# Optimization experiments

Hardware: AMD Instinct MI355X
Metric: run time of the kernel (lower is better)

The kernel has to match this reference:

```python
import jax, jax.numpy as jnp
import numpy as np

B, H, W, C, NH = 16, 56, 56, 192, 6
N = H * W
HD = C // NH
EPS = 1e-5


def _ln(x, g, b):
    m = jnp.mean(x, -1, keepdims=True)
    v = jnp.mean((x - m) ** 2, -1, keepdims=True)
    return (x - m) * jax.lax.rsqrt(v + EPS) * g + b


def _dwconv(x, w, b):
    # x: (B,H,W,Ch), w: (3,3,1,Ch) depthwise, SAME padding
    y = jax.lax.conv_general_dilated(
        x, w, (1, 1), 'SAME',
        dimension_numbers=('NHWC', 'HWIO', 'NHWC'),
        feature_group_count=x.shape[-1])
    return y + b


def _rope_tables():
    k_max = C // 4  # 2D RoPE: feature_dim // (2 * num_spatial_dims)
    theta = 1.0 / (10000.0 ** (jnp.arange(k_max, dtype=jnp.float32) / k_max))
    ai = jnp.arange(H, dtype=jnp.float32)[:, None, None] * theta
    aj = jnp.arange(W, dtype=jnp.float32)[None, :, None] * theta
    ang = jnp.concatenate([jnp.broadcast_to(ai, (H, W, k_max)),
                           jnp.broadcast_to(aj, (H, W, k_max))], -1)  # (H,W,C//2)
    return jnp.cos(ang), jnp.sin(ang)


def _rope(x, cos, sin):
    # x: (B,H,W,C); complex multiply on interleaved (re,im) pairs
    xr, xi = x[..., 0::2], x[..., 1::2]
    return jnp.stack([cos * xr - sin * xi, cos * xi + sin * xr], -1).reshape(x.shape)


def reference(x, cpe1_w, cpe1_b, norm1_g, norm1_b, in_w, in_b, actp_w, actp_b,
              dwc_w, dwc_b, qk_w, qk_b, lepe_w, lepe_b, outp_w, outp_b,
              cpe2_w, cpe2_b, norm2_g, norm2_b, fc1_w, fc1_b, mdw_w, mdw_b,
              fc2_w, fc2_b, mn1_g, mn1_b, mn2_g, mn2_b, mn3_g, mn3_b):
    img = lambda t: t.reshape(B, H, W, -1)
    seq = lambda t: t.reshape(B, N, -1)

    # CPE1
    x = x + seq(_dwconv(img(x), cpe1_w, cpe1_b))
    shortcut = x
    xn = _ln(x, norm1_g, norm1_b)

    # gated branch
    act_res = jax.nn.silu(xn @ actp_w + actp_b)
    h = seq(jax.nn.silu(_dwconv(img(xn @ in_w + in_b), dwc_w, dwc_b)))

    # --- LinearAttention (ELU+1 kernel, RoPE, LePE) ---
    qk = h @ qk_w + qk_b                      # (B,N,2C)
    q = jax.nn.elu(qk[..., :C]) + 1.0
    k = jax.nn.elu(qk[..., C:]) + 1.0
    cos, sin = _rope_tables()
    q_r = seq(_rope(img(q), cos, sin)).reshape(B, N, NH, HD)
    k_r = seq(_rope(img(k), cos, sin)).reshape(B, N, NH, HD)
    q4 = q.reshape(B, N, NH, HD)
    k4 = k.reshape(B, N, NH, HD)
    v4 = h.reshape(B, N, NH, HD)
    kmean = jnp.mean(k4, axis=1)                                  # (B,NH,HD)
    z = 1.0 / (jnp.einsum('bnhd,bhd->bnh', q4, kmean) + 1e-6)     # (B,N,NH)
    kv = jnp.einsum('bnhd,bnhe->bhde', k_r, v4) / N               # (B,NH,HD,HD)
    attn = jnp.einsum('bnhd,bhde->bnhe', q_r, kv) * z[..., None]
    attn = attn.reshape(B, N, C)
    attn = attn + seq(_dwconv(img(h), lepe_w, lepe_b))            # LePE on v

    x = shortcut + (attn * act_res) @ outp_w + outp_b

    # CPE2
    x = x + seq(_dwconv(img(x), cpe2_w, cpe2_b))

    # FRN MLP: fc1 -> dwconv -> 3 chained residual LayerNorms -> GELU -> fc2
    xm = _ln(x, norm2_g, norm2_b)
    f1 = xm @ fc1_w + fc1_b                   # (B,N,768)
    dw = seq(_dwconv(img(f1), mdw_w, mdw_b))
    n1 = _ln(dw + f1, mn1_g, mn1_b)
    n2 = _ln(n1 + f1, mn2_g, mn2_b)
    n3 = _ln(n2 + f1, mn3_g, mn3_b)
    x = x + jax.nn.gelu(n3, approximate=False) @ fc2_w + fc2_b
    return x


def setup_inputs() -> dict:
    key = jax.random.key(0)
    cnt = [0]
    def rn(shape, s=0.05):
        cnt[0] += 1
        return jax.random.normal(jax.random.fold_in(key, cnt[0]), shape, jnp.float32) * s
    dws = (3, 3, 1, C)
    z = lambda n: jnp.zeros((n,), jnp.float32)
    o = lambda n: jnp.ones((n,), jnp.float32)
    return dict(
        x=rn((B, N, C), 1.0),
        cpe1_w=rn(dws), cpe1_b=z(C),
        norm1_g=o(C), norm1_b=z(C),
        in_w=rn((C, C)), in_b=z(C),
        actp_w=rn((C, C)), actp_b=z(C),
        dwc_w=rn(dws), dwc_b=z(C),
        qk_w=rn((C, 2 * C)), qk_b=z(2 * C),
        lepe_w=rn(dws), lepe_b=z(C),
        outp_w=rn((C, C)), outp_b=z(C),
        cpe2_w=rn(dws), cpe2_b=z(C),
        norm2_g=o(C), norm2_b=z(C),
        fc1_w=rn((C, 4 * C)), fc1_b=z(4 * C),
        mdw_w=rn((3, 3, 1, 4 * C)), mdw_b=z(4 * C),
        fc2_w=rn((4 * C, C)), fc2_b=z(C),
        mn1_g=o(4 * C), mn1_b=z(4 * C),
        mn2_g=o(4 * C), mn2_b=z(4 * C),
        mn3_g=o(4 * C), mn3_b=z(4 * C),
    )
```

## Files before the change

kernel.cpp:

```cpp
#include <hip/hip_runtime.h>
#include <hip/hip_bf16.h>
#include <math.h>

#define BB 16
#define HH 56
#define WW 56
#define CC0 192
#define NHH 6
#define HDD 32
#define NPOS (HH*WW)
#define MROWS (BB*NPOS)
#define C4 (4*CC0)

typedef __hip_bfloat16 bf16;
typedef short short8 __attribute__((ext_vector_type(8)));
typedef short short4v __attribute__((ext_vector_type(4)));
typedef float f32x4 __attribute__((ext_vector_type(4)));
typedef float f32x2 __attribute__((ext_vector_type(2)));
typedef unsigned int u32;
typedef u32 u32x4 __attribute__((ext_vector_type(4)));
typedef u32 u32x2 __attribute__((ext_vector_type(2)));

__device__ __forceinline__ float b2f(bf16 v){ return __bfloat162float(v); }
__device__ __forceinline__ bf16 f2b(float v){ return __float2bfloat16(v); }
__device__ __forceinline__ short f2s(float v){ bf16 b = __float2bfloat16(v); return *(short*)&b; }
__device__ __forceinline__ float s2f(short s){ bf16 b; *(short*)&b = s; return __bfloat162float(b); }
__device__ __forceinline__ f32x2 bfp(u32 u){
  union { u32 q; float f; } lo, hi;
  lo.q = u << 16; hi.q = u & 0xffff0000u;
  return (f32x2){lo.f, hi.f};
}
__device__ __forceinline__ float fast_gelu(float x){
  float u = 1.5957691216f * (x + 0.044715f*x*x*x);
  float t = 1.f - 2.f/(__expf(u) + 1.f);
  return 0.5f*x*(1.f + t);
}
__device__ __forceinline__ int swz8(int bid, int nblk){
  return (bid & 7) * (nblk >> 3) + (bid >> 3);
}

__global__ __launch_bounds__(256) void convert_weights(
    const float* __restrict__ w0, const float* __restrict__ w1,
    const float* __restrict__ w2, const float* __restrict__ w3,
    const float* __restrict__ w4, const float* __restrict__ w5,
    short* __restrict__ dst){
  int t = blockIdx.x*256 + threadIdx.x;
  int e = t*4;
  if (e >= 479232) return;
  const float* src; int K, N, off;
  if      (e <  36864){ src=w0; K=192; N=192; off=0; }
  else if (e <  73728){ src=w1; K=192; N=192; off=36864; }
  else if (e < 147456){ src=w2; K=192; N=384; off=73728; }
  else if (e < 184320){ src=w3; K=192; N=192; off=147456; }
  else if (e < 331776){ src=w4; K=192; N=768; off=184320; }
  else                { src=w5; K=768; N=192; off=331776; }
  int le = e - off;
  int n = le / K, k = le % K;
  short4v o;
  #pragma unroll
  for (int l = 0; l < 4; ++l) o[l] = f2s(src[(size_t)(k+l)*N + n]);
  *(short4v*)(dst + e) = o;
}

__global__ __launch_bounds__(256) void cpe_ln_kernel(const float* __restrict__ in,
    const float* __restrict__ w, const float* __restrict__ bias,
    const float* __restrict__ g, const float* __restrict__ bb,
    float* __restrict__ x1out, bf16* __restrict__ xnout){
  int wv = threadIdx.x >> 6, lane = threadIdx.x & 63;
  int grp = swz8(blockIdx.x, gridDim.x)*4 + wv;
  int pos0 = grp * 4;
  int b = pos0 / NPOS; int ij = pos0 % NPOS; int i = ij / WW; int j0 = ij % WW;
  int c = lane * 3;
  float acc[4][3];
  {
    float b0 = bias[c], b1 = bias[c+1], b2 = bias[c+2];
    #pragma unroll
    for (int p = 0; p < 4; ++p){ acc[p][0]=b0; acc[p][1]=b1; acc[p][2]=b2; }
  }
  float fc[4][3];
  bool leftOK  = (j0 > 0);
  bool rightOK = (j0 + 4 < WW);
  int base_i = (b*NPOS + i*WW + j0)*CC0 + c;

  #pragma unroll
  for (int di = 0; di < 3; ++di){
    int ii = i + di - 1;
    if (ii < 0 || ii >= HH) continue;
    int rb = base_i + (di-1)*(WW*CC0);
    float wt[3][3];
    #pragma unroll
    for (int dj = 0; dj < 3; ++dj){
      const float* wp = w + (di*3 + dj)*CC0 + c;
      wt[dj][0] = wp[0]; wt[dj][1] = wp[1]; wt[dj][2] = wp[2];
    }
    if (leftOK){
      const float* ip = in + rb - CC0;
      float d0 = ip[0], d1 = ip[1], d2 = ip[2];
      acc[0][0] += d0*wt[0][0]; acc[0][1] += d1*wt[0][1]; acc[0][2] += d2*wt[0][2];
    }
    #pragma unroll
    for (int col = 1; col <= 4; ++col){
      const float* ip = in + rb + (col-1)*CC0;
      float d0 = ip[0], d1 = ip[1], d2 = ip[2];
      if (di == 1){ fc[col-1][0] = d0; fc[col-1][1] = d1; fc[col-1][2] = d2; }
      #pragma unroll
      for (int dj = 0; dj < 3; ++dj){
        int p = col - dj;
        if (p >= 0 && p < 4){
          acc[p][0] += d0*wt[dj][0]; acc[p][1] += d1*wt[dj][1]; acc[p][2] += d2*wt[dj][2];
        }
      }
    }
    if (rightOK){
      const float* ip = in + rb + 4*CC0;
      float d0 = ip[0], d1 = ip[1], d2 = ip[2];
      acc[3][0] += d0*wt[2][0]; acc[3][1] += d1*wt[2][1]; acc[3][2] += d2*wt[2][2];
    }
  }
  float gv0 = g[c], gv1 = g[c+1], gv2 = g[c+2];
  float bv0 = bb[c], bv1 = bb[c+1], bv2 = bb[c+2];
  #pragma unroll
  for (int p = 0; p < 4; ++p){
    float v0 = fc[p][0] + acc[p][0];
    float v1 = fc[p][1] + acc[p][1];
    float v2 = fc[p][2] + acc[p][2];
    int base = (pos0 + p)*CC0 + c;
    float* xp = x1out + base;
    xp[0] = v0; xp[1] = v1; xp[2] = v2;
    float s = v0+v1+v2, q = v0*v0+v1*v1+v2*v2;
    #pragma unroll
    for (int m = 1; m < 64; m <<= 1){ s += __shfl_xor(s, m, 64); q += __shfl_xor(q, m, 64); }
    float mean = s * (1.f/CC0);
    float rstd = rsqrtf(q * (1.f/CC0) - mean*mean + 1e-5f);
    bf16* op = xnout + base;
    op[0] = f2b((v0-mean)*rstd*gv0 + bv0);
    op[1] = f2b((v1-mean)*rstd*gv1 + bv1);
    op[2] = f2b((v2-mean)*rstd*gv2 + bv2);
  }
}

template<typename TIN, int CC, int MODE>
__global__ __launch_bounds__(256) void dwconv_v(const TIN* __restrict__ in,
    const float* __restrict__ w, const float* __restrict__ bias, void* __restrict__ out){
  constexpr int VEC = 16 / (int)sizeof(TIN);
  constexpr int NG = CC / VEC;
  int idx = swz8(blockIdx.x, gridDim.x)*256 + threadIdx.x;
  int cg = idx % NG; int pos = idx / NG;
  int b = pos / NPOS; int ij = pos % NPOS; int i = ij / WW; int j = ij % WW;
  int cb = cg * VEC;
  float acc[VEC];
  #pragma unroll
  for (int l = 0; l < VEC; ++l) acc[l] = bias[cb + l];
  #pragma unroll
  for (int di = 0; di < 3; ++di){
    int ii = i + di - 1;
    if (ii < 0 || ii >= HH) continue;
    #pragma unroll
    for (int dj = 0; dj < 3; ++dj){
      int jj = j + dj - 1;
      if (jj < 0 || jj >= WW) continue;
      int off = (b*NPOS + ii*WW + jj)*CC + cb;
      const float* wp = w + (di*3 + dj)*CC + cb;
      short8 v = *(const short8*)((const short*)in + off);
      #pragma unroll
      for (int l = 0; l < 8; ++l) acc[l] += s2f(v[l]) * wp[l];
    }
  }
  int oidx = pos*CC + cb;
  if constexpr (MODE == 1){
    short8 o;
    #pragma unroll
    for (int l = 0; l < 8; ++l){ float s = acc[l]/(1.f + expf(-acc[l])); o[l] = f2s(s); }
    *(short8*)((short*)out + oidx) = o;
  } else {
    short* op = (short*)out + oidx;
    short8 r = *(short8*)op;
    short8 o;
    #pragma unroll
    for (int l = 0; l < 8; ++l) o[l] = f2s(s2f(r[l]) + acc[l]);
    *(short8*)op = o;
  }
}

#define BM 256
#define BN 64
#define BK 32
#define LDA 40
template<int K, int N, int ALOAD, int EPI>
__global__ __launch_bounds__(256) void mfma_gemm(
    const void* __restrict__ a0v, const void* __restrict__ a1v,
    const short* __restrict__ wT, const float* __restrict__ bias,
    const float* __restrict__ addf, void* __restrict__ out0, void* __restrict__ out1){
  __shared__ short As[BM*LDA];
  __shared__ short Bs[BN*LDA];
  int tid = threadIdx.x;
  int wave = tid >> 6, lane = tid & 63;
  size_t m0 = (size_t)blockIdx.x * BM;
  int n0 = blockIdx.y * BN;
  int wm = wave * 64;
  int am = lane & 15, ak = (lane >> 4) * 8;

  f32x4 acc[4][4];
  #pragma unroll
  for (int mt = 0; mt < 4; ++mt)
    #pragma unroll
    for (int nt = 0; nt < 4; ++nt)
      acc[mt][nt] = (f32x4){0.f,0.f,0.f,0.f};

  for (int k0 = 0; k0 < K; k0 += BK){
    if constexpr (ALOAD == 0){
      const short* A = (const short*)a0v;
      #pragma unroll
      for (int it = 0; it < 4; ++it){
        int idx = it*256 + tid;
        int row = idx >> 2; int ko = (idx & 3) * 8;
        short8 v = *(const short8*)(A + (m0 + row)*(size_t)K + k0 + ko);
        *(short8*)&As[row*LDA + ko] = v;
      }
    } else {
      const short* A0p = (const short*)a0v;
      const short* A1p = (const short*)a1v;
      #pragma unroll
      for (int it = 0; it < 4; ++it){
        int idx = it*256 + tid;
        int row = idx >> 2; int ko = (idx & 3) * 8;
        size_t off = (m0 + row)*(size_t)K + k0 + ko;
        short8 va = *(const short8*)(A0p + off);
        short8 vb = *(const short8*)(A1p + off);
        short8 o;
        #pragma unroll
        for (int l = 0; l < 8; ++l) o[l] = f2s(s2f(va[l]) * s2f(vb[l]));
        *(short8*)&As[row*LDA + ko] = o;
      }
    }
    {
      int row = tid >> 2; int ko = (tid & 3) * 8;
      short8 v = *(const short8*)(wT + (size_t)(n0 + row)*K + k0 + ko);
      *(short8*)&Bs[row*LDA + ko] = v;
    }
    __syncthreads();
    short8 af[4], bfr[4];
    #pragma unroll
    for (int mt = 0; mt < 4; ++mt) af[mt] = *(short8*)&As[(wm + mt*16 + am)*LDA + ak];
    #pragma unroll
    for (int nt = 0; nt < 4; ++nt) bfr[nt] = *(short8*)&Bs[(nt*16 + am)*LDA + ak];
    #pragma unroll
    for (int mt = 0; mt < 4; ++mt)
      #pragma unroll
      for (int nt = 0; nt < 4; ++nt)
        acc[mt][nt] = __builtin_amdgcn_mfma_f32_16x16x32_bf16(af[mt], bfr[nt], acc[mt][nt], 0, 0, 0);
    __syncthreads();
  }

  int cn = lane & 15;
  int cr = (lane >> 4) * 4;
  #pragma unroll
  for (int mt = 0; mt < 4; ++mt){
    #pragma unroll
    for (int nt = 0; nt < 4; ++nt){
      int gn = n0 + nt*16 + cn;
      float bv = bias[gn];
      #pragma unroll
      for (int r = 0; r < 4; ++r){
        size_t gm = m0 + wm + mt*16 + cr + r;
        float v = acc[mt][nt][r] + bv;
        if constexpr (EPI == 0){
          ((bf16*)out0)[gm*N + gn] = f2b(v);
        } else if constexpr (EPI == 1){
          ((bf16*)out0)[gm*N + gn] = f2b(v / (1.f + expf(-v)));
        } else if constexpr (EPI == 2){
          float rv = (v > 0.f) ? (v + 1.f) : expf(v);
          if (n0 < CC0) ((bf16*)out0)[gm*CC0 + gn] = f2b(rv);
          else          ((bf16*)out1)[gm*CC0 + (gn - CC0)] = f2b(rv);
        } else {
          ((float*)out0)[gm*N + gn] = addf[gm*N + gn] + v;
        }
      }
    }
  }
}

__global__ void rope_tables_kernel(float* __restrict__ cosT, float* __restrict__ sinT){
  int idx = blockIdx.x*256 + threadIdx.x;
  if (idx >= NPOS*96) return;
  int t = idx % 96; int ij = idx / 96; int i = ij / WW; int j = ij % WW;
  int kk = (t < 48) ? t : (t - 48);
  float th = expf(-(float)kk * 0.19188209108283716f);
  float pos = (t < 48) ? (float)i : (float)j;
  float ang = pos * th;
  cosT[idx] = cosf(ang);
  sinT[idx] = sinf(ang);
}

__global__ __launch_bounds__(CC0) void kmean_kernel(const bf16* __restrict__ k, float* __restrict__ kmean){
  int b = blockIdx.x / 28; int chunk = blockIdx.x % 28; int c = threadIdx.x;
  const bf16* kp = k + ((size_t)b*NPOS + (size_t)chunk*112)*CC0 + c;
  float s0 = 0.f, s1 = 0.f, s2 = 0.f, s3 = 0.f;
  #pragma unroll 1
  for (int r = 0; r < 112; r += 4){
    s0 += b2f(kp[(size_t)(r+0)*CC0]);
    s1 += b2f(kp[(size_t)(r+1)*CC0]);
    s2 += b2f(kp[(size_t)(r+2)*CC0]);
    s3 += b2f(kp[(size_t)(r+3)*CC0]);
  }
  atomicAdd(&kmean[b*CC0 + c], (s0+s1+s2+s3) * (1.f/NPOS));
}

#define KVCH 14
__global__ __launch_bounds__(256) void kv_kernel(const bf16* __restrict__ kbuf,
    const bf16* __restrict__ hbuf, const float* __restrict__ cosT,
    const float* __restrict__ sinT, float* __restrict__ kv){
  int bi = blockIdx.x;
  int chunk = bi % KVCH; bi /= KVCH;
  int h = bi % NHH; int b = bi / NHH;
  int tid = threadIdx.x;
  int r8 = tid >> 5, lane = tid & 31;
  __shared__ float krs[8][32];
  __shared__ float vvs[8][32];
  int d = tid >> 3; int ebase = (tid & 7) * 4;
  float a0 = 0.f, a1 = 0.f, a2 = 0.f, a3 = 0.f;
  int c = h*HDD + lane;
  int t = c >> 1;
  bool odd = (lane & 1);
  for (int step = 0; step < NPOS/(KVCH*8); ++step){
    int n = chunk*(NPOS/KVCH) + step*8 + r8;
    size_t row = (size_t)b*NPOS + n;
    float kc = b2f(kbuf[row*CC0 + c]);
    float kp = b2f(kbuf[row*CC0 + (c ^ 1)]);
    float cs = cosT[(size_t)n*96 + t], sn = sinT[(size_t)n*96 + t];
    krs[r8][lane] = odd ? (cs*kc + sn*kp) : (cs*kc - sn*kp);
    vvs[r8][lane] = b2f(hbuf[row*CC0 + c]);
    __syncthreads();
    #pragma unroll
    for (int nn = 0; nn < 8; ++nn){
      float kk2 = krs[nn][d];
      a0 += kk2 * vvs[nn][ebase+0];
      a1 += kk2 * vvs[nn][ebase+1];
      a2 += kk2 * vvs[nn][ebase+2];
      a3 += kk2 * vvs[nn][ebase+3];
    }
    __syncthreads();
  }
  const float invN = 1.f/NPOS;
  float* kvp = kv + (((size_t)(b*NHH + h)*HDD + d)*HDD) + ebase;
  atomicAdd(kvp+0, a0*invN);
  atomicAdd(kvp+1, a1*invN);
  atomicAdd(kvp+2, a2*invN);
  atomicAdd(kvp+3, a3*invN);
}

__global__ __launch_bounds__(CC0) void attn_kernel(const bf16* __restrict__ q,
    const float* __restrict__ kmean, const float* __restrict__ kv,
    const float* __restrict__ cosT, const float* __restrict__ sinT,
    bf16* __restrict__ out){
  int row = blockIdx.x;
  int tid = threadIdx.x;
  int b = row / NPOS; int n = row % NPOS;
  __shared__ float qs[CC0];
  __shared__ float qrs[NHH*33];
  __shared__ float zsh[NHH];
  qs[tid] = b2f(q[(size_t)row*CC0 + tid]);
  __syncthreads();
  float pm = qs[tid] * kmean[b*CC0 + tid];
  #pragma unroll
  for (int m = 16; m >= 1; m >>= 1) pm += __shfl_xor(pm, m, 32);
  if ((tid & 31) == 0) zsh[tid >> 5] = 1.f/(pm + 1e-6f);
  int t = tid >> 1;
  float cs = cosT[(size_t)n*96 + t], sn = sinT[(size_t)n*96 + t];
  float qr = (tid & 1) ? (cs*qs[tid] + sn*qs[tid-1]) : (cs*qs[tid] - sn*qs[tid+1]);
  int hh = tid >> 5, d = tid & 31;
  qrs[hh*33 + d] = qr;
  __syncthreads();
  const float* kvp = kv + (size_t)(b*NHH + hh)*HDD*HDD;
  float acc = 0.f;
  #pragma unroll
  for (int d2 = 0; d2 < HDD; ++d2) acc += qrs[hh*33 + d2] * kvp[d2*HDD + d];
  out[(size_t)row*CC0 + tid] = f2b(acc * zsh[hh]);
}

__global__ __launch_bounds__(256) void mdw_ln_kernel(const bf16* __restrict__ f1,
    const float* __restrict__ w, const float* __restrict__ bias,
    const float* __restrict__ g1, const float* __restrict__ b1,
    const float* __restrict__ g2, const float* __restrict__ b2,
    const float* __restrict__ g3, const float* __restrict__ b3,
    bf16* __restrict__ out){
  int wv = threadIdx.x >> 6, lane = threadIdx.x & 63;
  int grp = swz8(blockIdx.x, gridDim.x)*4 + wv;
  int pos0 = grp * 4;
  int b = pos0 / NPOS; int ij = pos0 % NPOS; int i = ij / WW; int j0 = ij % WW;
  int c0 = lane * 8;
  int c1 = 512 + lane * 4;
  const short* fp = (const short*)f1;

  f32x2 acc2[4][6];
  {
    f32x2 bv[6];
    #pragma unroll
    for (int l = 0; l < 4; ++l) bv[l] = *(const f32x2*)(bias + c0 + 2*l);
    bv[4] = *(const f32x2*)(bias + c1);
    bv[5] = *(const f32x2*)(bias + c1 + 2);
    #pragma unroll
    for (int p = 0; p < 4; ++p)
      #pragma unroll
      for (int l = 0; l < 6; ++l) acc2[p][l] = bv[l];
  }
  u32x4 fca[4]; u32x2 fcb[4];
  bool leftOK  = (j0 > 0);
  bool rightOK = (j0 + 4 < WW);
  int base_i = (b*NPOS + i*WW + j0)*C4;

  #pragma unroll
  for (int di = 0; di < 3; ++di){
    int ii = i + di - 1;
    if (ii < 0 || ii >= HH) continue;
    int rb = base_i + (di-1)*(WW*C4);
    f32x2 wt2[3][6];
    #pragma unroll
    for (int dj = 0; dj < 3; ++dj){
      const float* wp = w + (di*3 + dj)*C4;
      #pragma unroll
      for (int l = 0; l < 4; ++l) wt2[dj][l] = *(const f32x2*)(wp + c0 + 2*l);
      wt2[dj][4] = *(const f32x2*)(wp + c1);
      wt2[dj][5] = *(const f32x2*)(wp + c1 + 2);
    }
    if (leftOK){
      u32x4 xa = *(const u32x4*)(fp + rb - C4 + c0);
      u32x2 xb = *(const u32x2*)(fp + rb - C4 + c1);
      f32x2 dv[6];
      dv[0]=bfp(xa[0]); dv[1]=bfp(xa[1]); dv[2]=bfp(xa[2]); dv[3]=bfp(xa[3]);
      dv[4]=bfp(xb[0]); dv[5]=bfp(xb[1]);
      #pragma unroll
      for (int l = 0; l < 6; ++l) acc2[0][l] += dv[l]*wt2[0][l];
    }
    #pragma unroll
    for (int col = 1; col <= 4; ++col){
      int off = rb + (col-1)*C4;
      u32x4 xa = *(const u32x4*)(fp + off + c0);
      u32x2 xb = *(const u32x2*)(fp + off + c1);
      if (di == 1){ fca[col-1] = xa; fcb[col-1] = xb; }
      f32x2 dv[6];
      dv[0]=bfp(xa[0]); dv[1]=bfp(xa[1]); dv[2]=bfp(xa[2]); dv[3]=bfp(xa[3]);
      dv[4]=bfp(xb[0]); dv[5]=bfp(xb[1]);
      #pragma unroll
      for (int dj = 0; dj < 3; ++dj){
        int p = col - dj;
        if (p >= 0 && p < 4){
          #pragma unroll
          for (int l = 0; l < 6; ++l) acc2[p][l] += dv[l]*wt2[dj][l];
        }
      }
    }
    if (rightOK){
      u32x4 xa = *(const u32x4*)(fp + rb + 4*C4 + c0);
      u32x2 xb = *(const u32x2*)(fp + rb + 4*C4 + c1);
      f32x2 dv[6];
      dv[0]=bfp(xa[0]); dv[1]=bfp(xa[1]); dv[2]=bfp(xa[2]); dv[3]=bfp(xa[3]);
      dv[4]=bfp(xb[0]); dv[5]=bfp(xb[1]);
      #pragma unroll
      for (int l = 0; l < 6; ++l) acc2[3][l] += dv[l]*wt2[2][l];
    }
  }
  #pragma unroll
  for (int p = 0; p < 4; ++p){
    #pragma unroll
    for (int l = 0; l < 4; ++l) acc2[p][l] += bfp(fca[p][l]);
    acc2[p][4] += bfp(fcb[p][0]);
    acc2[p][5] += bfp(fcb[p][1]);
  }

  const float* gs[3] = {g1, g2, g3};
  const float* bs[3] = {b1, b2, b3};
  #pragma unroll
  for (int pass = 0; pass < 3; ++pass){
    f32x2 gv[6], bvv[6];
    #pragma unroll
    for (int l = 0; l < 4; ++l){
      gv[l]  = *(const f32x2*)(gs[pass] + c0 + 2*l);
      bvv[l] = *(const f32x2*)(bs[pass] + c0 + 2*l);
    }
    gv[4]  = *(const f32x2*)(gs[pass] + c1);  gv[5]  = *(const f32x2*)(gs[pass] + c1 + 2);
    bvv[4] = *(const f32x2*)(bs[pass] + c1);  bvv[5] = *(const f32x2*)(bs[pass] + c1 + 2);
    #pragma unroll
    for (int p = 0; p < 4; ++p){
      f32x2 s2 = acc2[p][0];
      f32x2 q2 = acc2[p][0]*acc2[p][0];
      #pragma unroll
      for (int l = 1; l < 6; ++l){ s2 += acc2[p][l]; q2 += acc2[p][l]*acc2[p][l]; }
      float s = s2[0]+s2[1], q = q2[0]+q2[1];
      #pragma unroll
      for (int m = 1; m < 64; m <<= 1){ s += __shfl_xor(s, m, 64); q += __shfl_xor(q, m, 64); }
      float mean = s * (1.f/C4);
      float rstd = rsqrtf(q * (1.f/C4) - mean*mean + 1e-5f);
      #pragma unroll
      for (int l = 0; l < 6; ++l){
        f32x2 rg = gv[l]*rstd;
        f32x2 t  = acc2[p][l] - mean;
        acc2[p][l] = t*rg + bvv[l];
      }
      if (pass < 2){
        #pragma unroll
        for (int l = 0; l < 4; ++l) acc2[p][l] += bfp(fca[p][l]);
        acc2[p][4] += bfp(fcb[p][0]);
        acc2[p][5] += bfp(fcb[p][1]);
      }
    }
  }
  #pragma unroll
  for (int p = 0; p < 4; ++p){
    short8 o0; short4v o1;
    #pragma unroll
    for (int l = 0; l < 4; ++l){
      o0[2*l]   = f2s(fast_gelu(acc2[p][l][0]));
      o0[2*l+1] = f2s(fast_gelu(acc2[p][l][1]));
    }
    o1[0] = f2s(fast_gelu(acc2[p][4][0]));
    o1[1] = f2s(fast_gelu(acc2[p][4][1]));
    o1[2] = f2s(fast_gelu(acc2[p][5][0]));
    o1[3] = f2s(fast_gelu(acc2[p][5][1]));
    int ob = (pos0 + p)*C4;
    *(short8*)((short*)out + ob + c0) = o0;
    *(short4v*)((short*)out + ob + c1) = o1;
  }
}

extern "C" void kernel_launch(void* const* d_in, const int* in_sizes, int n_in,
                              void* d_out, int out_size, void* d_ws, size_t ws_size,
                              hipStream_t stream){
  (void)in_sizes; (void)n_in; (void)out_size; (void)ws_size;
  const float* X      = (const float*)d_in[0];
  const float* cpe1_w = (const float*)d_in[1];
  const float* cpe1_b = (const float*)d_in[2];
  const float* n1g    = (const float*)d_in[3];
  const float* n1b    = (const float*)d_in[4];
  const float* in_w   = (const float*)d_in[5];
  const float* in_b   = (const float*)d_in[6];
  const float* actp_w = (const float*)d_in[7];
  const float* actp_b = (const float*)d_in[8];
  const float* dwc_w  = (const float*)d_in[9];
  const float* dwc_b  = (const float*)d_in[10];
  const float* qk_w   = (const float*)d_in[11];
  const float* qk_b   = (const float*)d_in[12];
  const float* lepe_w = (const float*)d_in[13];
  const float* lepe_b = (const float*)d_in[14];
  const float* outp_w = (const float*)d_in[15];
  const float* outp_b = (const float*)d_in[16];
  const float* cpe2_w = (const float*)d_in[17];
  const float* cpe2_b = (const float*)d_in[18];
  const float* n2g    = (const float*)d_in[19];
  const float* n2b    = (const float*)d_in[20];
  const float* fc1_w  = (const float*)d_in[21];
  const float* fc1_b  = (const float*)d_in[22];
  const float* mdw_w  = (const float*)d_in[23];
  const float* mdw_b  = (const float*)d_in[24];
  const float* fc2_w  = (const float*)d_in[25];
  const float* fc2_b  = (const float*)d_in[26];
  const float* mn1g   = (const float*)d_in[27];
  const float* mn1b   = (const float*)d_in[28];
  const float* mn2g   = (const float*)d_in[29];
  const float* mn2b   = (const float*)d_in[30];
  const float* mn3g   = (const float*)d_in[31];
  const float* mn3b   = (const float*)d_in[32];

  char* ws = (char*)d_ws;
  const size_t SZF = (size_t)MROWS*CC0*4;
  const size_t SZB = (size_t)MROWS*CC0*2;
  float* A0 = (float*)(ws);
  char* base2 = ws + SZF;
  bf16* BQ = (bf16*)(base2 + 0*SZB);
  bf16* BKb= (bf16*)(base2 + 1*SZB);
  bf16* BA = (bf16*)(base2 + 2*SZB);
  bf16* B1 = (bf16*)(base2 + 3*SZB);
  bf16* B0 = (bf16*)(base2 + 4*SZB);
  bf16* B2 = (bf16*)(base2 + 5*SZB);
  bf16* B3 = (bf16*)(base2 + 6*SZB);
  float* A1 = (float*)(base2);
  bf16*  F1 = (bf16*)(base2);
  bf16*  DW = (bf16*)(base2 + 4*SZB);
  short* WT = (short*)(base2 + 8*SZB);
  char* tail = (char*)(WT + 479232 + 64);
  float* KMEAN = (float*)tail;                 tail += (size_t)BB*CC0*4;
  float* KV    = (float*)tail;                 tail += (size_t)BB*NHH*HDD*HDD*4;
  float* COS   = (float*)tail;                 tail += (size_t)NPOS*96*4;
  float* SIN   = (float*)tail;

  const short* actpT = WT + 0;
  const short* inT   = WT + 36864;
  const short* qkT   = WT + 73728;
  const short* outpT = WT + 147456;
  const short* fc1T  = WT + 184320;
  const short* fc2T  = WT + 331776;

  const int G192B = (MROWS*(CC0/8))/256;
  const int GPOS16 = MROWS/16;

  convert_weights<<<(479232/4 + 255)/256, 256, 0, stream>>>(actp_w, in_w, qk_w, outp_w, fc1_w, fc2_w, WT);
  rope_tables_kernel<<<(NPOS*96 + 255)/256, 256, 0, stream>>>(COS, SIN);
  cpe_ln_kernel<<<GPOS16, 256, 0, stream>>>(X, cpe1_w, cpe1_b, n1g, n1b, A0, B0);
  mfma_gemm<CC0,CC0,0,1><<<dim3(MROWS/BM,CC0/BN), 256, 0, stream>>>(B0, nullptr, actpT, actp_b, nullptr, B1, nullptr);
  mfma_gemm<CC0,CC0,0,0><<<dim3(MROWS/BM,CC0/BN), 256, 0, stream>>>(B0, nullptr, inT, in_b, nullptr, B2, nullptr);
  dwconv_v<bf16,CC0,1><<<G192B, 256, 0, stream>>>(B2, dwc_w, dwc_b, B3);
  mfma_gemm<CC0,2*CC0,0,2><<<dim3(MROWS/BM,2*CC0/BN), 256, 0, stream>>>(B3, nullptr, qkT, qk_b, nullptr, BQ, BKb);
  hipMemsetAsync(KMEAN, 0, (size_t)BB*CC0*4, stream);
  hipMemsetAsync(KV, 0, (size_t)BB*NHH*HDD*HDD*4, stream);
  kmean_kernel<<<BB*28, CC0, 0, stream>>>(BKb, KMEAN);
  kv_kernel<<<BB*NHH*KVCH, 256, 0, stream>>>(BKb, B3, COS, SIN, KV);
  attn_kernel<<<MROWS, CC0, 0, stream>>>(BQ, KMEAN, KV, COS, SIN, BA);
  dwconv_v<bf16,CC0,2><<<G192B, 256, 0, stream>>>(B3, lepe_w, lepe_b, BA);
  mfma_gemm<CC0,CC0,1,3><<<dim3(MROWS/BM,CC0/BN), 256, 0, stream>>>(BA, B1, outpT, outp_b, A0, A1, nullptr);
  cpe_ln_kernel<<<GPOS16, 256, 0, stream>>>(A1, cpe2_w, cpe2_b, n2g, n2b, A0, B0);
  mfma_gemm<CC0,C4,0,0><<<dim3(MROWS/BM,C4/BN), 256, 0, stream>>>(B0, nullptr, fc1T, fc1_b, nullptr, F1, nullptr);
  mdw_ln_kernel<<<GPOS16, 256, 0, stream>>>(F1, mdw_w, mdw_b, mn1g, mn1b, mn2g, mn2b, mn3g, mn3b, DW);
  mfma_gemm<C4,CC0,0,3><<<dim3(MROWS/BM,CC0/BN), 256, 0, stream>>>(DW, nullptr, fc2T, fc2_b, A0, d_out, nullptr);
}
```

Measured before the change: 625.0 us.

## Fuse actp and in_proj GEMMs and register-block depthwise conv over four columns

```diff
diff --git a/kernel.cpp b/kernel.cpp
--- a/kernel.cpp
+++ b/kernel.cpp
@@ -139,46 +139,86 @@
   }
 }
 
-template<typename TIN, int CC, int MODE>
-__global__ __launch_bounds__(256) void dwconv_v(const TIN* __restrict__ in,
+template<int MODE>
+__global__ __launch_bounds__(256) void dwconv4(const bf16* __restrict__ in,
     const float* __restrict__ w, const float* __restrict__ bias, void* __restrict__ out){
-  constexpr int VEC = 16 / (int)sizeof(TIN);
-  constexpr int NG = CC / VEC;
   int idx = swz8(blockIdx.x, gridDim.x)*256 + threadIdx.x;
-  int cg = idx % NG; int pos = idx / NG;
-  int b = pos / NPOS; int ij = pos % NPOS; int i = ij / WW; int j = ij % WW;
-  int cb = cg * VEC;
-  float acc[VEC];
-  #pragma unroll
-  for (int l = 0; l < VEC; ++l) acc[l] = bias[cb + l];
+  int cg = idx % 24; int quad = idx / 24;
+  int pos0 = quad * 4;
+  int b = pos0 / NPOS; int ij = pos0 % NPOS; int i = ij / WW; int j0 = ij % WW;
+  int cb = cg * 8;
+  const short* fp = (const short*)in;
+  f32x2 acc[4][4];
+  {
+    f32x2 bv0 = *(const f32x2*)(bias + cb);
+    f32x2 bv1 = *(const f32x2*)(bias + cb + 2);
+    f32x2 bv2 = *(const f32x2*)(bias + cb + 4);
+    f32x2 bv3 = *(const f32x2*)(bias + cb + 6);
+    #pragma unroll
+    for (int p = 0; p < 4; ++p){ acc[p][0]=bv0; acc[p][1]=bv1; acc[p][2]=bv2; acc[p][3]=bv3; }
+  }
+  bool leftOK  = (j0 > 0);
+  bool rightOK = (j0 + 4 < WW);
+  int base_i = (b*NPOS + i*WW + j0)*CC0 + cb;
+
   #pragma unroll
   for (int di = 0; di < 3; ++di){
     int ii = i + di - 1;
     if (ii < 0 || ii >= HH) continue;
+    int rb = base_i + (di-1)*(WW*CC0);
+    const float* wr = w + (di*3)*CC0 + cb;
+    f32x2 wt[3][4];
     #pragma unroll
     for (int dj = 0; dj < 3; ++dj){
-      int jj = j + dj - 1;
-      if (jj < 0 || jj >= WW) continue;
-      int off = (b*NPOS + ii*WW + jj)*CC + cb;
-      const float* wp = w + (di*3 + dj)*CC + cb;
-      short8 v = *(const short8*)((const short*)in + off);
-      #pragma unroll
-      for (int l = 0; l < 8; ++l) acc[l] += s2f(v[l]) * wp[l];
-    }
-  }
-  int oidx = pos*CC + cb;
-  if constexpr (MODE == 1){
+      #pragma unroll
+      for (int l = 0; l < 4; ++l) wt[dj][l] = *(const f32x2*)(wr + dj*CC0 + 2*l);
+    }
+    if (leftOK){
+      u32x4 x = *(const u32x4*)(fp + rb - CC0);
+      #pragma unroll
+      for (int l = 0; l < 4; ++l) acc[0][l] += bfp(x[l])*wt[0][l];
+    }
+    #pragma unroll
+    for (int col = 1; col <= 4; ++col){
+      u32x4 x = *(const u32x4*)(fp + rb + (col-1)*CC0);
+      f32x2 dv[4];
+      #pragma unroll
+      for (int l = 0; l < 4; ++l) dv[l] = bfp(x[l]);
+      #pragma unroll
+      for (int dj = 0; dj < 3; ++dj){
+        int p = col - dj;
+        if (p >= 0 && p < 4){
+          #pragma unroll
+          for (int l = 0; l < 4; ++l) acc[p][l] += dv[l]*wt[dj][l];
+        }
+      }
+    }
+    if (rightOK){
+      u32x4 x = *(const u32x4*)(fp + rb + 4*CC0);
+      #pragma unroll
+      for (int l = 0; l < 4; ++l) acc[3][l] += bfp(x[l])*wt[2][l];
+    }
+  }
+  #pragma unroll
+  for (int p = 0; p < 4; ++p){
+    int oidx = (pos0 + p)*CC0 + cb;
     short8 o;
-    #pragma unroll
-    for (int l = 0; l < 8; ++l){ float s = acc[l]/(1.f + expf(-acc[l])); o[l] = f2s(s); }
+    if constexpr (MODE == 1){
+      #pragma unroll
+      for (int l = 0; l < 4; ++l){
+        float a0 = acc[p][l][0], a1 = acc[p][l][1];
+        o[2*l]   = f2s(a0/(1.f + expf(-a0)));
+        o[2*l+1] = f2s(a1/(1.f + expf(-a1)));
+      }
+    } else {
+      u32x4 r = *(const u32x4*)((const short*)out + oidx);
+      #pragma unroll
+      for (int l = 0; l < 4; ++l){
+        f32x2 s = bfp(r[l]) + acc[p][l];
+        o[2*l] = f2s(s[0]); o[2*l+1] = f2s(s[1]);
+      }
+    }
     *(short8*)((short*)out + oidx) = o;
-  } else {
-    short* op = (short*)out + oidx;
-    short8 r = *(short8*)op;
-    short8 o;
-    #pragma unroll
-    for (int l = 0; l < 8; ++l) o[l] = f2s(s2f(r[l]) + acc[l]);
-    *(short8*)op = o;
   }
 }
 
@@ -259,7 +299,9 @@
     #pragma unroll
     for (int nt = 0; nt < 4; ++nt){
       int gn = n0 + nt*16 + cn;
-      float bv = bias[gn];
+      float bv;
+      if constexpr (EPI == 4) bv = (n0 < CC0) ? bias[gn] : addf[gn - CC0];
+      else bv = bias[gn];
       #pragma unroll
       for (int r = 0; r < 4; ++r){
         size_t gm = m0 + wm + mt*16 + cr + r;
@@ -272,6 +314,9 @@
           float rv = (v > 0.f) ? (v + 1.f) : expf(v);
           if (n0 < CC0) ((bf16*)out0)[gm*CC0 + gn] = f2b(rv);
           else          ((bf16*)out1)[gm*CC0 + (gn - CC0)] = f2b(rv);
+        } else if constexpr (EPI == 4){
+          if (n0 < CC0) ((bf16*)out0)[gm*CC0 + gn] = f2b(v / (1.f + expf(-v)));
+          else          ((bf16*)out1)[gm*CC0 + (gn - CC0)] = f2b(v);
         } else {
           ((float*)out0)[gm*N + gn] = addf[gm*N + gn] + v;
         }
@@ -584,28 +629,26 @@
   float* SIN   = (float*)tail;
 
   const short* actpT = WT + 0;
-  const short* inT   = WT + 36864;
   const short* qkT   = WT + 73728;
   const short* outpT = WT + 147456;
   const short* fc1T  = WT + 184320;
   const short* fc2T  = WT + 331776;
 
-  const int G192B = (MROWS*(CC0/8))/256;
   const int GPOS16 = MROWS/16;
+  const int GDW4   = (MROWS/4)*24/256;
 
   convert_weights<<<(479232/4 + 255)/256, 256, 0, stream>>>(actp_w, in_w, qk_w, outp_w, fc1_w, fc2_w, WT);
   rope_tables_kernel<<<(NPOS*96 + 255)/256, 256, 0, stream>>>(COS, SIN);
   cpe_ln_kernel<<<GPOS16, 256, 0, stream>>>(X, cpe1_w, cpe1_b, n1g, n1b, A0, B0);
-  mfma_gemm<CC0,CC0,0,1><<<dim3(MROWS/BM,CC0/BN), 256, 0, stream>>>(B0, nullptr, actpT, actp_b, nullptr, B1, nullptr);
-  mfma_gemm<CC0,CC0,0,0><<<dim3(MROWS/BM,CC0/BN), 256, 0, stream>>>(B0, nullptr, inT, in_b, nullptr, B2, nullptr);
-  dwconv_v<bf16,CC0,1><<<G192B, 256, 0, stream>>>(B2, dwc_w, dwc_b, B3);
+  mfma_gemm<CC0,2*CC0,0,4><<<dim3(MROWS/BM,2*CC0/BN), 256, 0, stream>>>(B0, nullptr, actpT, actp_b, in_b, B1, B2);
+  dwconv4<1><<<GDW4, 256, 0, stream>>>(B2, dwc_w, dwc_b, B3);
   mfma_gemm<CC0,2*CC0,0,2><<<dim3(MROWS/BM,2*CC0/BN), 256, 0, stream>>>(B3, nullptr, qkT, qk_b, nullptr, BQ, BKb);
   hipMemsetAsync(KMEAN, 0, (size_t)BB*CC0*4, stream);
   hipMemsetAsync(KV, 0, (size_t)BB*NHH*HDD*HDD*4, stream);
   kmean_kernel<<<BB*28, CC0, 0, stream>>>(BKb, KMEAN);
   kv_kernel<<<BB*NHH*KVCH, 256, 0, stream>>>(BKb, B3, COS, SIN, KV);
   attn_kernel<<<MROWS, CC0, 0, stream>>>(BQ, KMEAN, KV, COS, SIN, BA);
-  dwconv_v<bf16,CC0,2><<<G192B, 256, 0, stream>>>(B3, lepe_w, lepe_b, BA);
+  dwconv4<2><<<GDW4, 256, 0, stream>>>(B3, lepe_w, lepe_b, BA);
   mfma_gemm<CC0,CC0,1,3><<<dim3(MROWS/BM,CC0/BN), 256, 0, stream>>>(BA, B1, outpT, outp_b, A0, A1, nullptr);
   cpe_ln_kernel<<<GPOS16, 256, 0, stream>>>(A1, cpe2_w, cpe2_b, n2g, n2b, A0, B0);
   mfma_gemm<CC0,C4,0,0><<<dim3(MROWS/BM,C4/BN), 256, 0, stream>>>(B0, nullptr, fc1T, fc1_b, nullptr, F1, nullptr);
```

Result: slower. 734.9 us (+17.6%).
